# Performance work log

Hardware: AMD Instinct MI355X
Metric: run time of the kernel (lower is better)

The kernel has to match this reference:

```python
import jax, jax.numpy as jnp
import numpy as np

B, T, DIM, MDIM, HID = 16, 2048, 1024, 128, 512
WIN = 16
HALF = WIN // 2              # 8 even / 8 odd tokens per window
MAXP = int(0.8 * HALF)       # candidate_ratio * min(nA, nB) = 6 pairs per window
SIM_THRESH = -10.0           # permissive: never masks a cosine similarity
KEEP_RATIO = 0.7
SIM_W, IMP_W, ALPHA_SCALE = 1.0, 0.5, 5.0
LN_EPS = 1e-5


def _ln(x, g, b):
    mu = jnp.mean(x, -1, keepdims=True)
    var = jnp.mean((x - mu) ** 2, -1, keepdims=True)
    return (x - mu) / jnp.sqrt(var + LN_EPS) * g + b


def _greedy(s):
    # s: [HALF, HALF] bipartite sims. Greedy conflict-free matching by descending
    # similarity; since min(nA,nB)=8 >= MAXP=6 it always yields exactly MAXP pairs.
    order = jnp.argsort(-s.reshape(-1))

    def body(k, st):
        usedA, usedB, pa, pb, cnt = st
        idx = order[k]
        iA = (idx // HALF).astype(jnp.int32)
        iB = (idx % HALF).astype(jnp.int32)
        ok = (cnt < MAXP) & (~usedA[iA]) & (~usedB[iB])
        usedA = usedA.at[iA].set(usedA[iA] | ok)
        usedB = usedB.at[iB].set(usedB[iB] | ok)
        w = jnp.where(ok, cnt, MAXP)  # slot MAXP is a scratch slot
        pa = pa.at[w].set(jnp.where(ok, iA, pa[w]))
        pb = pb.at[w].set(jnp.where(ok, iB, pb[w]))
        return (usedA, usedB, pa, pb, cnt + ok.astype(jnp.int32))

    st0 = (jnp.zeros(HALF, bool), jnp.zeros(HALF, bool),
           jnp.zeros(MAXP + 1, jnp.int32), jnp.zeros(MAXP + 1, jnp.int32),
           jnp.int32(0))
    _, _, pa, pb, _ = jax.lax.fori_loop(0, HALF * HALF, body, st0)
    pa, pb = pa[:MAXP], pb[:MAXP]
    return pa, pb, s[pa, pb]


def _forward(x, ln_m_g, ln_m_b, w_match, ln_i_g, ln_i_b, w_imp1, b_imp1, w_imp2, b_imp2):
    Bc, Tc, C = x.shape
    nW = Tc // WIN
    P = nW * MAXP
    K = int((1.0 - KEEP_RATIO) * Tc)  # fixed merge budget (top-K)

    # matching space (L2-normalized) and per-token importance
    m = _ln(x, ln_m_g, ln_m_b) @ w_match                      # [B,T,MDIM]
    m = m / jnp.linalg.norm(m, axis=-1, keepdims=True)
    h = jax.nn.relu(_ln(x, ln_i_g, ln_i_b) @ w_imp1 + b_imp1)
    imp = jax.nn.sigmoid((h @ w_imp2 + b_imp2)[..., 0])       # [B,T]

    # windowed even/odd bipartite similarity
    mw = m.reshape(Bc, nW, WIN, MDIM)
    sim = jnp.einsum('bwad,bwcd->bwac', mw[:, :, 0::2], mw[:, :, 1::2])  # [B,nW,8,8]
    sim = jnp.where(sim < SIM_THRESH, -jnp.inf, sim)

    pa, pb, sv = jax.vmap(jax.vmap(_greedy))(sim)             # [B,nW,MAXP]
    wstart = (jnp.arange(nW, dtype=jnp.int32) * WIN)[None, :, None]
    i_idx = (wstart + 2 * pa).reshape(Bc, P)                  # keep token (even)
    j_idx = (wstart + 2 * pb + 1).reshape(Bc, P)              # drop token (odd)
    sim_c = sv.reshape(Bc, P)
    imp_i = jnp.take_along_axis(imp, i_idx, axis=1)
    imp_j = jnp.take_along_axis(imp, j_idx, axis=1)

    # fixed budget: exactly top-K merges by score (high sim, low importance)
    scores = SIM_W * sim_c - IMP_W * 0.5 * (imp_i + imp_j)
    _, top = jax.lax.top_k(scores, K)
    z = jnp.zeros((Bc, P), x.dtype).at[jnp.arange(Bc)[:, None], top].set(1.0)

    # merge keeps i, drops j; alpha from relative importance
    alpha = jax.nn.sigmoid(ALPHA_SCALE * (imp_i - imp_j))[..., None]
    xi = jnp.take_along_axis(x, i_idx[..., None], axis=1)
    xj = jnp.take_along_axis(x, j_idx[..., None], axis=1)
    merged = alpha * xi + (1.0 - alpha) * xj                  # [B,P,C]

    def pack_one(xb, ib, jb, mb, zb):
        # i indices are globally unique -> scatter merged content where z==1
        x_new = xb.at[ib].add(zb[:, None] * (mb - xb[ib]))
        drop = (jnp.zeros(Tc, xb.dtype).at[jb].add(zb)) > 0.5
        # stable argsort keeps surviving tokens in time order; take first T-K
        order = jnp.argsort(drop.astype(jnp.int32))[:Tc - K]
        return x_new[order]

    return jax.vmap(pack_one)(x, i_idx, j_idx, merged, z)     # [B, T-K, C]


def setup_inputs() -> dict:
    key = jax.random.key(0)
    ks = jax.random.split(key, 4)
    s = 0.02
    return {
        'x': jax.random.normal(ks[0], (B, T, DIM), jnp.float32),
        'ln_m_g': jnp.ones((DIM,), jnp.float32),
        'ln_m_b': jnp.zeros((DIM,), jnp.float32),
        'w_match': jax.random.normal(ks[1], (DIM, MDIM), jnp.float32) * s,
        'ln_i_g': jnp.ones((DIM,), jnp.float32),
        'ln_i_b': jnp.zeros((DIM,), jnp.float32),
        'w_imp1': jax.random.normal(ks[2], (DIM, HID), jnp.float32) * s,
        'b_imp1': jnp.zeros((HID,), jnp.float32),
        'w_imp2': jax.random.normal(ks[3], (HID, 1), jnp.float32) * s,
        'b_imp2': jnp.zeros((1,), jnp.float32),
    }


def reference(x, ln_m_g, ln_m_b, w_match, ln_i_g, ln_i_b, w_imp1, b_imp1, w_imp2, b_imp2):
    return _forward(x, ln_m_g, ln_m_b, w_match, ln_i_g, ln_i_b, w_imp1, b_imp1, w_imp2, b_imp2)
```

## Files before the change

kernel.cpp:

```cpp
#include <hip/hip_runtime.h>
#include <math.h>

#define B_ 16
#define T_ 2048
#define DIM_ 1024
#define MDIM_ 128
#define HID_ 512
#define NCAT 640
#define NW_ 128
#define WINSZ 16
#define MAXP_ 6
#define P_ 768
#define KDROP 614
#define TKEEP 1434
#define NTOK (B_*T_)

typedef unsigned short u16;
typedef __bf16 bf16x8 __attribute__((ext_vector_type(8)));
typedef float f32x4 __attribute__((ext_vector_type(4)));
typedef unsigned short us4 __attribute__((ext_vector_type(4)));

#define OFF_WCAT   0
#define OFF_BIAS   (OFF_WCAT + DIM_*NCAT)
#define OFF_MU     (OFF_BIAS + NCAT)
#define OFF_RS     (OFF_MU + NTOK)
#define OFF_MBUF   (OFF_RS + NTOK)
#define OFF_LOGIT  (OFF_MBUF + NTOK*MDIM_)
#define OFF_IIDX   (OFF_LOGIT + NTOK)
#define OFF_JIDX   (OFF_IIDX + B_*P_)
#define OFF_SV     (OFF_JIDX + B_*P_)
#define OFF_ALPHA  (OFF_SV + B_*P_)
#define OFF_REP    (OFF_ALPHA + B_*P_)
#define OFF_DROP   (OFF_REP + NTOK)
#define OFF_POS    (OFF_DROP + NTOK)

static constexpr size_t F_AH    = 0;
static constexpr size_t F_AL    = F_AH + (size_t)NTOK*DIM_/2;
static constexpr size_t F_BH    = F_AL + (size_t)NTOK*DIM_/2;
static constexpr size_t F_BL    = F_BH + (size_t)NCAT*DIM_/2;
static constexpr size_t F_BIAS  = F_BL + (size_t)NCAT*DIM_/2;
static constexpr size_t F_MBUF  = F_BIAS + NCAT;
static constexpr size_t F_LOGIT = F_MBUF + (size_t)NTOK*MDIM_;
static constexpr size_t F_IIDX  = F_LOGIT + NTOK;
static constexpr size_t F_JIDX  = F_IIDX + (size_t)B_*P_;
static constexpr size_t F_SV    = F_JIDX + (size_t)B_*P_;
static constexpr size_t F_ALPHA = F_SV + (size_t)B_*P_;
static constexpr size_t F_REP   = F_ALPHA + (size_t)B_*P_;
static constexpr size_t F_DROP  = F_REP + NTOK;
static constexpr size_t F_POS   = F_DROP + NTOK;
static constexpr size_t F_TOTAL = F_POS + NTOK;

__device__ __forceinline__ u16 f2bf(float f) {
  unsigned u = __builtin_bit_cast(unsigned, f);
  unsigned r = u + 0x7FFFu + ((u >> 16) & 1u);
  return (u16)(r >> 16);
}
__device__ __forceinline__ float bf2f(u16 h) {
  unsigned u = ((unsigned)h) << 16;
  return __builtin_bit_cast(float, u);
}
__device__ __forceinline__ void gll16(const void* g, void* l) {
  __builtin_amdgcn_global_load_lds((const __attribute__((address_space(1))) void*)g,
                                   (__attribute__((address_space(3))) void*)l, 16, 0, 0);
}


#define NBLK_A (NTOK / 4)
#define NBLK_B ((NCAT * DIM_) / 256)
__global__ __launch_bounds__(256) void prep_all(const float* __restrict__ x,
    const float* __restrict__ wm, const float* __restrict__ wi,
    const float* __restrict__ gm, const float* __restrict__ gi,
    const float* __restrict__ bm, const float* __restrict__ bi,
    const float* __restrict__ b1,
    u16* __restrict__ Ah, u16* __restrict__ Al,
    u16* __restrict__ Bh, u16* __restrict__ Bl,
    float* __restrict__ biascat, float* __restrict__ logit) {
  int bid = blockIdx.x;
  if (bid < NBLK_A) {
    int token = bid * 4 + (threadIdx.x >> 6);
    int lane = threadIdx.x & 63;
    if (lane == 0) logit[token] = 0.f;
    const float4* xr = (const float4*)(x + (size_t)token * DIM_);
    float4 v[4];
    float sum = 0.f;
#pragma unroll
    for (int it = 0; it < 4; ++it) {
      v[it] = xr[lane + it * 64];
      sum += v[it].x + v[it].y + v[it].z + v[it].w;
    }
    for (int o = 32; o > 0; o >>= 1) sum += __shfl_xor(sum, o);
    float m = sum * (1.f / 1024.f);
    float ss = 0.f;
#pragma unroll
    for (int it = 0; it < 4; ++it) {
      float a = v[it].x - m, b = v[it].y - m, c = v[it].z - m, d = v[it].w - m;
      ss += a * a + b * b + c * c + d * d;
    }
    for (int o = 32; o > 0; o >>= 1) ss += __shfl_xor(ss, o);
    float rsv = 1.0f / sqrtf(ss * (1.f / 1024.f) + 1e-5f);
#pragma unroll
    for (int it = 0; it < 4; ++it) {
      float e[4] = {(v[it].x - m) * rsv, (v[it].y - m) * rsv,
                    (v[it].z - m) * rsv, (v[it].w - m) * rsv};
      us4 hv, lv;
#pragma unroll
      for (int j = 0; j < 4; ++j) {
        u16 h = f2bf(e[j]);
        hv[j] = h;
        lv[j] = f2bf(e[j] - bf2f(h));
      }
      size_t off = (size_t)token * DIM_ + (size_t)(lane + it * 64) * 4;
      *(us4*)&Ah[off] = hv;
      *(us4*)&Al[off] = lv;
    }
  } else if (bid < NBLK_A + NBLK_B) {
    int e = (bid - NBLK_A) * 256 + threadIdx.x;
    int n = e >> 10, k = e & 1023;
    float wv = (n < MDIM_) ? gm[k] * wm[k * MDIM_ + n]
                           : gi[k] * wi[k * HID_ + (n - MDIM_)];
    u16 h = f2bf(wv);
    Bh[e] = h;
    Bl[e] = f2bf(wv - bf2f(h));
  } else {
    int c = bid - NBLK_A - NBLK_B;
    float s = 0.f;
    for (int k = threadIdx.x; k < DIM_; k += 256)
      s += (c < MDIM_) ? bm[k] * wm[k * MDIM_ + c]
                       : bi[k] * wi[k * HID_ + (c - MDIM_)];
    __shared__ float red[256];
    red[threadIdx.x] = s; __syncthreads();
    for (int o = 128; o > 0; o >>= 1) {
      if (threadIdx.x < o) red[threadIdx.x] += red[threadIdx.x + o];
      __syncthreads();
    }
    if (threadIdx.x == 0)
      biascat[c] = red[0] + ((c >= MDIM_) ? b1[c - MDIM_] : 0.f);
  }
}

__global__ __launch_bounds__(256, 2) void gemm_mfma(
    const u16* __restrict__ Ah, const u16* __restrict__ Al,
    const u16* __restrict__ Bh, const u16* __restrict__ Bl,
    const float* __restrict__ biascat, const float* __restrict__ w2,
    float* __restrict__ mbuf, float* __restrict__ logit) {
  __shared__ __align__(16) u16 sAH[2][8 * 512];
  __shared__ __align__(16) u16 sAL[2][8 * 512];
  __shared__ __align__(16) u16 sBH[2][8 * 512];
  __shared__ __align__(16) u16 sBL[2][8 * 512];
  const int tid = threadIdx.x;
  const int w = tid >> 6, lane = tid & 63;
  int bid = blockIdx.x;
  int q = bid / 40, rem = bid % 40;
  int ct = rem >> 3, x8 = rem & 7;
  int stripe = x8 + 8 * q;
  const int row0 = stripe * 128, col0 = ct * 128;
  const int wy = w >> 1, wx = w & 1;
  const int m16 = lane & 15, quad = lane >> 4;

  const u16* gA = (w == 0) ? Ah : (w == 1) ? Al : (w == 2) ? Bh : Bl;
  u16* lds0 = ((w == 0) ? sAH[0] : (w == 1) ? sAL[0] : (w == 2) ? sBH[0] : sBL[0]) + lane * 8;
  u16* lds1 = ((w == 0) ? sAH[1] : (w == 1) ? sAL[1] : (w == 2) ? sBH[1] : sBL[1]) + lane * 8;
  const int rbase = (w < 2) ? row0 : col0;
  const u16* gsrc0 = gA + (size_t)(rbase + m16) * DIM_ + quad * 8;

#pragma unroll
  for (int t = 0; t < 8; ++t)
    gll16(gsrc0 + (size_t)t * 16 * DIM_, lds0 + t * 512);
#pragma unroll
  for (int t = 0; t < 8; ++t)
    gll16(gsrc0 + (size_t)t * 16 * DIM_ + 32, lds1 + t * 512);
  __builtin_amdgcn_sched_barrier(0);
  asm volatile("s_waitcnt vmcnt(8)" ::: "memory");
  __builtin_amdgcn_s_barrier();
  __builtin_amdgcn_sched_barrier(0);

  f32x4 acc[4][4] = {};
  for (int k0 = 0; k0 < 32; ++k0) {
    const int cb = k0 & 1;
    bf16x8 ah[4], al[4], bh[4], bl[4];
#pragma unroll
    for (int i = 0; i < 4; ++i) {
      ah[i] = *(const bf16x8*)&sAH[cb][(wy * 4 + i) * 512 + lane * 8];
      al[i] = *(const bf16x8*)&sAL[cb][(wy * 4 + i) * 512 + lane * 8];
      bh[i] = *(const bf16x8*)&sBH[cb][(wx * 4 + i) * 512 + lane * 8];
      bl[i] = *(const bf16x8*)&sBL[cb][(wx * 4 + i) * 512 + lane * 8];
    }
    __builtin_amdgcn_sched_barrier(0);
    asm volatile("s_waitcnt lgkmcnt(0)" ::: "memory");
    __builtin_amdgcn_sched_barrier(0);
    __builtin_amdgcn_s_barrier();
    __builtin_amdgcn_sched_barrier(0);
    if (k0 + 2 < 32) {
      u16* nb = cb ? lds1 : lds0;
#pragma unroll
      for (int t = 0; t < 8; ++t)
        gll16(gsrc0 + (size_t)t * 16 * DIM_ + (k0 + 2) * 32, nb + t * 512);
    }
    __builtin_amdgcn_sched_barrier(0);
#pragma unroll
    for (int i = 0; i < 4; ++i)
#pragma unroll
      for (int j = 0; j < 4; ++j) {
        acc[i][j] = __builtin_amdgcn_mfma_f32_16x16x32_bf16(ah[i], bh[j], acc[i][j], 0, 0, 0);
        acc[i][j] = __builtin_amdgcn_mfma_f32_16x16x32_bf16(ah[i], bl[j], acc[i][j], 0, 0, 0);
        acc[i][j] = __builtin_amdgcn_mfma_f32_16x16x32_bf16(al[i], bh[j], acc[i][j], 0, 0, 0);
      }
    __builtin_amdgcn_sched_barrier(0);
    if (k0 < 30) {
      asm volatile("s_waitcnt vmcnt(8)" ::: "memory");
    } else {
      asm volatile("s_waitcnt vmcnt(0)" ::: "memory");
    }
    __builtin_amdgcn_s_barrier();
    __builtin_amdgcn_sched_barrier(0);
  }
  if (ct == 0) {
#pragma unroll
    for (int i = 0; i < 4; ++i)
#pragma unroll
      for (int j = 0; j < 4; ++j) {
        int col = wx * 64 + j * 16 + m16;
        float bs = biascat[col];
#pragma unroll
        for (int r = 0; r < 4; ++r) {
          int row = row0 + wy * 64 + i * 16 + quad * 4 + r;
          mbuf[(size_t)row * MDIM_ + col] = acc[i][j][r] + bs;
        }
      }
  } else {
#pragma unroll
    for (int i = 0; i < 4; ++i) {
      float part[4] = {0.f, 0.f, 0.f, 0.f};
#pragma unroll
      for (int j = 0; j < 4; ++j) {
        int col = col0 + wx * 64 + j * 16 + m16;
        float bs = biascat[col];
        float wv = w2[col - MDIM_];
#pragma unroll
        for (int r = 0; r < 4; ++r) {
          float v = acc[i][j][r] + bs;
          v = v > 0.f ? v : 0.f;
          part[r] += v * wv;
        }
      }
#pragma unroll
      for (int r = 0; r < 4; ++r) {
        part[r] += __shfl_xor(part[r], 1);
        part[r] += __shfl_xor(part[r], 2);
        part[r] += __shfl_xor(part[r], 4);
        part[r] += __shfl_xor(part[r], 8);
      }
      if (m16 == 0)
#pragma unroll
        for (int r = 0; r < 4; ++r)
          atomicAdd(&logit[row0 + wy * 64 + i * 16 + quad * 4 + r], part[r]);
    }
  }
}


__global__ __launch_bounds__(256) void simgreedy(const float* __restrict__ mbuf,
    int* __restrict__ ii, int* __restrict__ jj, float* __restrict__ sv) {
  __shared__ __align__(16) float sm[4][16][132];
  int wv = threadIdx.x >> 6, lane = threadIdx.x & 63;
  int win = blockIdx.x * 4 + wv;
  int b = win >> 7, w = win & 127;
  size_t base = ((size_t)b * T_ + w * WINSZ) * MDIM_;
#pragma unroll
  for (int it = 0; it < 8; ++it) {
    int e4 = it * 64 + lane;
    int row = e4 >> 5, c4 = e4 & 31;
    float4 v = *(const float4*)(mbuf + base + (size_t)row * MDIM_ + c4 * 4);
    *(float4*)&sm[wv][row][c4 * 4] = v;
  }
  __syncthreads();
  {
    int row = lane >> 2, seg = lane & 3;
    float* r = sm[wv][row] + seg * 32;
    float ss = 0.f;
#pragma unroll
    for (int k = 0; k < 32; ++k) ss += r[k] * r[k];
    ss += __shfl_xor(ss, 1);
    ss += __shfl_xor(ss, 2);
    float inv = 1.0f / sqrtf(ss);
#pragma unroll
    for (int k = 0; k < 32; ++k) r[k] *= inv;
  }
  __syncthreads();
  int a = lane >> 3, c = lane & 7;
  const float* ev = sm[wv][2 * a];
  const float* od = sm[wv][2 * c + 1];
  float s = 0.f;
#pragma unroll
  for (int k = 0; k < MDIM_; ++k) s += ev[k] * od[k];
  if (s < -10.0f) s = -__builtin_inff();
  float v = s;
  bool alive = true;
  int outb = (b * NW_ + w) * MAXP_;
  for (int p = 0; p < MAXP_; ++p) {
    float bv = alive ? v : -__builtin_inff();
    int bi = lane;
    for (int o = 32; o > 0; o >>= 1) {
      float ov = __shfl_xor(bv, o);
      int oi = __shfl_xor(bi, o);
      if (ov > bv || (ov == bv && oi < bi)) { bv = ov; bi = oi; }
    }
    int wa = bi >> 3, wc = bi & 7;
    if (lane == 0) {
      ii[outb + p] = w * WINSZ + 2 * wa;
      jj[outb + p] = w * WINSZ + 2 * wc + 1;
      sv[outb + p] = bv;
    }
    if (a == wa || c == wc) alive = false;
  }
}

__global__ __launch_bounds__(1024) void select_fused(const float* __restrict__ sv,
    const int* __restrict__ ii, const int* __restrict__ jj,
    const float* __restrict__ logit, const float* __restrict__ b2,
    float* __restrict__ alpha, int* __restrict__ rep,
    int* __restrict__ drop, int* __restrict__ pos) {
  int b = blockIdx.x, tid = threadIdx.x;
  __shared__ float sc[P_];
  __shared__ int sdrop[T_];
  __shared__ int wtot[16];
  float bb = b2[0];
  for (int t = tid; t < T_; t += 1024) {
    sdrop[t] = 0;
    rep[b * T_ + t] = -1;
  }
  if (tid < P_) {
    int i = ii[b * P_ + tid], j = jj[b * P_ + tid];
    float fi = 1.f / (1.f + expf(-(logit[b * T_ + i] + bb)));
    float fj = 1.f / (1.f + expf(-(logit[b * T_ + j] + bb)));
    sc[tid] = sv[b * P_ + tid] - 0.25f * (fi + fj);
    alpha[b * P_ + tid] = 1.f / (1.f + expf(-5.f * (fi - fj)));
  }
  __syncthreads();
  if (tid < P_) {
    float s = sc[tid];
    int cnt = 0;
    for (int qq = 0; qq < P_; ++qq) {
      float t = sc[qq];
      cnt += (t > s) || (t == s && qq < tid);
    }
    if (cnt < KDROP) {
      rep[b * T_ + ii[b * P_ + tid]] = tid;
      sdrop[jj[b * P_ + tid]] = 1;
    }
  }
  __syncthreads();
  int base = tid * 2;
  int loc0 = 0;
  int loc1 = (sdrop[base] ? 0 : 1);
  int s = loc1 + (sdrop[base + 1] ? 0 : 1);
  int lane = tid & 63, wvi = tid >> 6;
  int incl = s;
  for (int o = 1; o < 64; o <<= 1) {
    int n = __shfl_up(incl, o);
    if (lane >= o) incl += n;
  }
  if (lane == 63) wtot[wvi] = incl;
  __syncthreads();
  int carry = 0;
  for (int ww = 0; ww < wvi; ++ww) carry += wtot[ww];
  int excl = carry + incl - s;
  drop[b * T_ + base] = sdrop[base];
  drop[b * T_ + base + 1] = sdrop[base + 1];
  pos[b * T_ + base] = excl + loc0;
  pos[b * T_ + base + 1] = excl + loc1;
}

__global__ __launch_bounds__(256) void pack_kernel(const float* __restrict__ x,
    const int* __restrict__ drop, const int* __restrict__ pos,
    const int* __restrict__ rep, const float* __restrict__ alpha,
    const int* __restrict__ jj, float* __restrict__ out) {
  int t = blockIdx.x, b = blockIdx.y;
  if (drop[b * T_ + t]) return;
  int tid = threadIdx.x;
  const float4* xi = (const float4*)(x + ((size_t)b * T_ + t) * DIM_);
  float4 v = xi[tid];
  int p = rep[b * T_ + t];
  if (p >= 0) {
    float a = alpha[b * P_ + p];
    int j = jj[b * P_ + p];
    const float4* xj = (const float4*)(x + ((size_t)b * T_ + j) * DIM_);
    float4 vj = xj[tid];
    v.x = a * v.x + (1.f - a) * vj.x;
    v.y = a * v.y + (1.f - a) * vj.y;
    v.z = a * v.z + (1.f - a) * vj.z;
    v.w = a * v.w + (1.f - a) * vj.w;
  }
  int np = pos[b * T_ + t];
  ((float4*)(out + ((size_t)b * TKEEP + np) * DIM_))[tid] = v;
}


__global__ __launch_bounds__(256) void build_wcat(const float* __restrict__ wm,
    const float* __restrict__ wi, const float* __restrict__ gm,
    const float* __restrict__ gi, float* __restrict__ Wcat) {
  int e = blockIdx.x * 256 + threadIdx.x;
  if (e >= DIM_ * NCAT) return;
  int k = e / NCAT, c = e - k * NCAT;
  float v = (c < MDIM_) ? gm[k] * wm[k * MDIM_ + c]
                        : gi[k] * wi[k * HID_ + (c - MDIM_)];
  Wcat[e] = v;
}

__global__ __launch_bounds__(256) void build_bias(const float* __restrict__ wm,
    const float* __restrict__ wi, const float* __restrict__ bm,
    const float* __restrict__ bi, const float* __restrict__ b1,
    float* __restrict__ biascat) {
  int c = blockIdx.x;
  float s = 0.f;
  for (int k = threadIdx.x; k < DIM_; k += 256)
    s += (c < MDIM_) ? bm[k] * wm[k * MDIM_ + c]
                     : bi[k] * wi[k * HID_ + (c - MDIM_)];
  __shared__ float red[256];
  red[threadIdx.x] = s; __syncthreads();
  for (int o = 128; o > 0; o >>= 1) {
    if (threadIdx.x < o) red[threadIdx.x] += red[threadIdx.x + o];
    __syncthreads();
  }
  if (threadIdx.x == 0)
    biascat[c] = red[0] + ((c >= MDIM_) ? b1[c - MDIM_] : 0.f);
}

__global__ __launch_bounds__(256) void ln_stats(const float* __restrict__ x,
    float* __restrict__ mu, float* __restrict__ rs) {
  int token = blockIdx.x * 4 + (threadIdx.x >> 6);
  int lane = threadIdx.x & 63;
  const float4* xr = (const float4*)(x + (size_t)token * DIM_);
  float4 v[4];
  float sum = 0.f;
#pragma unroll
  for (int it = 0; it < 4; ++it) {
    v[it] = xr[lane + it * 64];
    sum += v[it].x + v[it].y + v[it].z + v[it].w;
  }
  for (int o = 32; o > 0; o >>= 1) sum += __shfl_xor(sum, o);
  float m = sum * (1.f / 1024.f);
  float ss = 0.f;
#pragma unroll
  for (int it = 0; it < 4; ++it) {
    float a = v[it].x - m, b = v[it].y - m, c = v[it].z - m, d = v[it].w - m;
    ss += a * a + b * b + c * c + d * d;
  }
  for (int o = 32; o > 0; o >>= 1) ss += __shfl_xor(ss, o);
  if (lane == 0) {
    mu[token] = m;
    rs[token] = 1.0f / sqrtf(ss * (1.f / 1024.f) + 1e-5f);
  }
}

__global__ __launch_bounds__(256) void gemm640(const float* __restrict__ x,
    const float* __restrict__ mu, const float* __restrict__ rs,
    const float* __restrict__ Wcat, const float* __restrict__ biascat,
    const float* __restrict__ w2, float* __restrict__ mbuf,
    float* __restrict__ logit) {
  __shared__ __align__(16) float As[16][68];
  __shared__ __align__(16) float Bs[16][68];
  const int tid = threadIdx.x;
  const int row0 = blockIdx.x * 64, col0 = blockIdx.y * 64;
  const int tx = tid & 15, ty = tid >> 4;
  const int arow = tid >> 2, akk = (tid & 3) << 2;
  const int brow = tid >> 4, bnn = (tid & 15) << 2;
  const int t_g = row0 + arow;
  const float tmu = mu[t_g], trs = rs[t_g];
  const float* xrow = x + (size_t)t_g * DIM_ + akk;
  const float* wptr = Wcat + (size_t)brow * NCAT + col0 + bnn;
  float acc[4][4] = {};
  for (int k0 = 0; k0 < DIM_; k0 += 16) {
    float4 av = *(const float4*)(xrow + k0);
    float4 bv = *(const float4*)(wptr + (size_t)k0 * NCAT);
    As[akk + 0][arow] = (av.x - tmu) * trs;
    As[akk + 1][arow] = (av.y - tmu) * trs;
    As[akk + 2][arow] = (av.z - tmu) * trs;
    As[akk + 3][arow] = (av.w - tmu) * trs;
    *(float4*)&Bs[brow][bnn] = bv;
    __syncthreads();
#pragma unroll
    for (int k = 0; k < 16; ++k) {
      float4 a = *(const float4*)&As[k][ty << 2];
      float4 b = *(const float4*)&Bs[k][tx << 2];
      acc[0][0] += a.x * b.x; acc[0][1] += a.x * b.y; acc[0][2] += a.x * b.z; acc[0][3] += a.x * b.w;
      acc[1][0] += a.y * b.x; acc[1][1] += a.y * b.y; acc[1][2] += a.y * b.z; acc[1][3] += a.y * b.w;
      acc[2][0] += a.z * b.x; acc[2][1] += a.z * b.y; acc[2][2] += a.z * b.z; acc[2][3] += a.z * b.w;
      acc[3][0] += a.w * b.x; acc[3][1] += a.w * b.y; acc[3][2] += a.w * b.z; acc[3][3] += a.w * b.w;
    }
    __syncthreads();
  }
  float bias[4];
#pragma unroll
  for (int j = 0; j < 4; ++j) bias[j] = biascat[col0 + (tx << 2) + j];
  if (col0 < MDIM_) {
#pragma unroll
    for (int i = 0; i < 4; ++i) {
      int t = row0 + (ty << 2) + i;
      float4 o;
      o.x = acc[i][0] + bias[0]; o.y = acc[i][1] + bias[1];
      o.z = acc[i][2] + bias[2]; o.w = acc[i][3] + bias[3];
      *(float4*)(mbuf + (size_t)t * MDIM_ + col0 + (tx << 2)) = o;
    }
  } else {
    float w2v[4];
#pragma unroll
    for (int j = 0; j < 4; ++j) w2v[j] = w2[col0 - MDIM_ + (tx << 2) + j];
#pragma unroll
    for (int i = 0; i < 4; ++i) {
      float p = 0.f;
#pragma unroll
      for (int j = 0; j < 4; ++j) {
        float v = acc[i][j] + bias[j];
        v = v > 0.f ? v : 0.f;
        p += v * w2v[j];
      }
      p += __shfl_xor(p, 1); p += __shfl_xor(p, 2);
      p += __shfl_xor(p, 4); p += __shfl_xor(p, 8);
      if (tx == 0) atomicAdd(&logit[row0 + (ty << 2) + i], p);
    }
  }
}

extern "C" void kernel_launch(void* const* d_in, const int* in_sizes, int n_in,
                              void* d_out, int out_size, void* d_ws, size_t ws_size,
                              hipStream_t stream) {
  const float* x    = (const float*)d_in[0];
  const float* gm   = (const float*)d_in[1];
  const float* bm   = (const float*)d_in[2];
  const float* wm   = (const float*)d_in[3];
  const float* gi   = (const float*)d_in[4];
  const float* bi   = (const float*)d_in[5];
  const float* wi   = (const float*)d_in[6];
  const float* b1   = (const float*)d_in[7];
  const float* w2   = (const float*)d_in[8];
  const float* b2   = (const float*)d_in[9];
  float* ws = (float*)d_ws;
  float* out = (float*)d_out;

  if (ws_size >= F_TOTAL * sizeof(float)) {
    u16* Ah = (u16*)(ws + F_AH);
    u16* Al = (u16*)(ws + F_AL);
    u16* Bh = (u16*)(ws + F_BH);
    u16* Bl = (u16*)(ws + F_BL);
    float* bias  = ws + F_BIAS;
    float* mbuf  = ws + F_MBUF;
    float* logit = ws + F_LOGIT;
    int* iidx    = (int*)(ws + F_IIDX);
    int* jidx    = (int*)(ws + F_JIDX);
    float* sv    = ws + F_SV;
    float* alpha = ws + F_ALPHA;
    int* rep     = (int*)(ws + F_REP);
    int* drop    = (int*)(ws + F_DROP);
    int* pos     = (int*)(ws + F_POS);

    prep_all<<<NBLK_A + NBLK_B + NCAT, 256, 0, stream>>>(
        x, wm, wi, gm, gi, bm, bi, b1, Ah, Al, Bh, Bl, bias, logit);
    gemm_mfma<<<(NTOK / 128) * (NCAT / 128), 256, 0, stream>>>(Ah, Al, Bh, Bl, bias, w2, mbuf, logit);
    simgreedy<<<(B_ * NW_) / 4, 256, 0, stream>>>(mbuf, iidx, jidx, sv);
    select_fused<<<B_, 1024, 0, stream>>>(sv, iidx, jidx, logit, b2, alpha, rep, drop, pos);
    dim3 pgrid(T_, B_);
    pack_kernel<<<pgrid, 256, 0, stream>>>(x, drop, pos, rep, alpha, jidx, out);
  } else {
    float* Wcat = ws + OFF_WCAT;
    float* bias = ws + OFF_BIAS;
    float* mu   = ws + OFF_MU;
    float* rs   = ws + OFF_RS;
    float* mbuf = ws + OFF_MBUF;
    float* logit = ws + OFF_LOGIT;
    int* iidx   = (int*)(ws + OFF_IIDX);
    int* jidx   = (int*)(ws + OFF_JIDX);
    float* sv   = ws + OFF_SV;
    float* alpha = ws + OFF_ALPHA;
    int* rep    = (int*)(ws + OFF_REP);
    int* drop   = (int*)(ws + OFF_DROP);
    int* pos    = (int*)(ws + OFF_POS);

    hipMemsetAsync(logit, 0, NTOK * sizeof(float), stream);
    build_wcat<<<(DIM_ * NCAT + 255) / 256, 256, 0, stream>>>(wm, wi, gm, gi, Wcat);
    build_bias<<<NCAT, 256, 0, stream>>>(wm, wi, bm, bi, b1, bias);
    ln_stats<<<NTOK / 4, 256, 0, stream>>>(x, mu, rs);
    dim3 ggrid(NTOK / 64, NCAT / 64);
    gemm640<<<ggrid, 256, 0, stream>>>(x, mu, rs, Wcat, bias, w2, mbuf, logit);
    simgreedy<<<(B_ * NW_) / 4, 256, 0, stream>>>(mbuf, iidx, jidx, sv);
    select_fused<<<B_, 1024, 0, stream>>>(sv, iidx, jidx, logit, b2, alpha, rep, drop, pos);
    dim3 pgrid(T_, B_);
    pack_kernel<<<pgrid, 256, 0, stream>>>(x, drop, pos, rep, alpha, jidx, out);
  }
}
```

Measured before the change: 475.2 us.

## Fuse windowed similarity and greedy matching into GEMM epilogue

The matching-space tile (ct==0 blocks) is now staged in LDS instead of written to a global mbuf. The same block then L2-normalizes rows, computes the even/odd 8x8 similarities per window and runs the greedy 6-pair selection with wave shuffles. This removes the mbuf round trip through global memory and the separate simgreedy launch. In exchange, only the 1-in-5 ct==0 blocks carry the extra epilogue work, LDS per block grows slightly (33792 u16 for the padded C tile), and the greedy order relies on argmax with index tie-breaking.

```diff
diff --git a/kernel.cpp b/kernel.cpp
--- a/kernel.cpp
+++ b/kernel.cpp
@@ -142,11 +142,14 @@
     const u16* __restrict__ Ah, const u16* __restrict__ Al,
     const u16* __restrict__ Bh, const u16* __restrict__ Bl,
     const float* __restrict__ biascat, const float* __restrict__ w2,
-    float* __restrict__ mbuf, float* __restrict__ logit) {
-  __shared__ __align__(16) u16 sAH[2][8 * 512];
-  __shared__ __align__(16) u16 sAL[2][8 * 512];
-  __shared__ __align__(16) u16 sBH[2][8 * 512];
-  __shared__ __align__(16) u16 sBL[2][8 * 512];
+    int* __restrict__ ii, int* __restrict__ jj, float* __restrict__ sv,
+    float* __restrict__ logit) {
+  __shared__ __align__(16) u16 smem[33792];
+  u16* sAH = smem;
+  u16* sAL = smem + 8192;
+  u16* sBH = smem + 16384;
+  u16* sBL = smem + 24576;
+  float* smC = (float*)smem;
   const int tid = threadIdx.x;
   const int w = tid >> 6, lane = tid & 63;
   int bid = blockIdx.x;
@@ -158,8 +161,8 @@
   const int m16 = lane & 15, quad = lane >> 4;
 
   const u16* gA = (w == 0) ? Ah : (w == 1) ? Al : (w == 2) ? Bh : Bl;
-  u16* lds0 = ((w == 0) ? sAH[0] : (w == 1) ? sAL[0] : (w == 2) ? sBH[0] : sBL[0]) + lane * 8;
-  u16* lds1 = ((w == 0) ? sAH[1] : (w == 1) ? sAL[1] : (w == 2) ? sBH[1] : sBL[1]) + lane * 8;
+  u16* lds0 = ((w == 0) ? sAH : (w == 1) ? sAL : (w == 2) ? sBH : sBL) + lane * 8;
+  u16* lds1 = lds0 + 4096;
   const int rbase = (w < 2) ? row0 : col0;
   const u16* gsrc0 = gA + (size_t)(rbase + m16) * DIM_ + quad * 8;
 
@@ -180,10 +183,10 @@
     bf16x8 ah[4], al[4], bh[4], bl[4];
 #pragma unroll
     for (int i = 0; i < 4; ++i) {
-      ah[i] = *(const bf16x8*)&sAH[cb][(wy * 4 + i) * 512 + lane * 8];
-      al[i] = *(const bf16x8*)&sAL[cb][(wy * 4 + i) * 512 + lane * 8];
-      bh[i] = *(const bf16x8*)&sBH[cb][(wx * 4 + i) * 512 + lane * 8];
-      bl[i] = *(const bf16x8*)&sBL[cb][(wx * 4 + i) * 512 + lane * 8];
+      ah[i] = *(const bf16x8*)&sAH[cb * 4096 + (wy * 4 + i) * 512 + lane * 8];
+      al[i] = *(const bf16x8*)&sAL[cb * 4096 + (wy * 4 + i) * 512 + lane * 8];
+      bh[i] = *(const bf16x8*)&sBH[cb * 4096 + (wx * 4 + i) * 512 + lane * 8];
+      bl[i] = *(const bf16x8*)&sBL[cb * 4096 + (wx * 4 + i) * 512 + lane * 8];
     }
     __builtin_amdgcn_sched_barrier(0);
     asm volatile("s_waitcnt lgkmcnt(0)" ::: "memory");
@@ -223,10 +226,56 @@
         float bs = biascat[col];
 #pragma unroll
         for (int r = 0; r < 4; ++r) {
-          int row = row0 + wy * 64 + i * 16 + quad * 4 + r;
-          mbuf[(size_t)row * MDIM_ + col] = acc[i][j][r] + bs;
+          int lr = wy * 64 + i * 16 + quad * 4 + r;
+          smC[lr * 132 + col] = acc[i][j][r] + bs;
         }
       }
+    __syncthreads();
+    const int bB = row0 >> 11;
+    const int wbase = (row0 & 2047) >> 4;
+    for (int ww = 0; ww < 2; ++ww) {
+      const int wi2 = w * 2 + ww;
+      float* wrow = &smC[wi2 * 16 * 132];
+      {
+        int row = lane >> 2, seg = lane & 3;
+        float* r = wrow + row * 132 + seg * 32;
+        float ss = 0.f;
+#pragma unroll
+        for (int k = 0; k < 32; ++k) ss += r[k] * r[k];
+        ss += __shfl_xor(ss, 1);
+        ss += __shfl_xor(ss, 2);
+        float inv = 1.0f / sqrtf(ss);
+#pragma unroll
+        for (int k = 0; k < 32; ++k) r[k] *= inv;
+      }
+      int a = lane >> 3, c = lane & 7;
+      const float* ev = wrow + (2 * a) * 132;
+      const float* od = wrow + (2 * c + 1) * 132;
+      float s = 0.f;
+#pragma unroll
+      for (int k = 0; k < MDIM_; ++k) s += ev[k] * od[k];
+      if (s < -10.0f) s = -__builtin_inff();
+      float v = s;
+      bool alive = true;
+      const int wtok = (wbase + wi2) * WINSZ;
+      const int outb = (bB * NW_ + wbase + wi2) * MAXP_;
+      for (int p = 0; p < MAXP_; ++p) {
+        float bv = alive ? v : -__builtin_inff();
+        int bi = lane;
+        for (int o = 32; o > 0; o >>= 1) {
+          float ov = __shfl_xor(bv, o);
+          int oi = __shfl_xor(bi, o);
+          if (ov > bv || (ov == bv && oi < bi)) { bv = ov; bi = oi; }
+        }
+        int wa = bi >> 3, wc = bi & 7;
+        if (lane == 0) {
+          ii[outb + p] = wtok + 2 * wa;
+          jj[outb + p] = wtok + 2 * wc + 1;
+          sv[outb + p] = bv;
+        }
+        if (a == wa || c == wc) alive = false;
+      }
+    }
   } else {
 #pragma unroll
     for (int i = 0; i < 4; ++i) {
@@ -544,7 +593,6 @@
     u16* Bh = (u16*)(ws + F_BH);
     u16* Bl = (u16*)(ws + F_BL);
     float* bias  = ws + F_BIAS;
-    float* mbuf  = ws + F_MBUF;
     float* logit = ws + F_LOGIT;
     int* iidx    = (int*)(ws + F_IIDX);
     int* jidx    = (int*)(ws + F_JIDX);
@@ -556,8 +604,8 @@
 
     prep_all<<<NBLK_A + NBLK_B + NCAT, 256, 0, stream>>>(
         x, wm, wi, gm, gi, bm, bi, b1, Ah, Al, Bh, Bl, bias, logit);
-    gemm_mfma<<<(NTOK / 128) * (NCAT / 128), 256, 0, stream>>>(Ah, Al, Bh, Bl, bias, w2, mbuf, logit);
-    simgreedy<<<(B_ * NW_) / 4, 256, 0, stream>>>(mbuf, iidx, jidx, sv);
+    gemm_mfma<<<(NTOK / 128) * (NCAT / 128), 256, 0, stream>>>(
+        Ah, Al, Bh, Bl, bias, w2, iidx, jidx, sv, logit);
     select_fused<<<B_, 1024, 0, stream>>>(sv, iidx, jidx, logit, b2, alpha, rep, drop, pos);
     dim3 pgrid(T_, B_);
     pack_kernel<<<pgrid, 256, 0, stream>>>(x, drop, pos, rep, alpha, jidx, out);
```

After: 475.4 us. No clear change (+0.1%).
